# Performance work log

Measured on AMD Instinct MI355X. Metric: run time of the kernel, lower is better.

The kernel has to match this reference:

```python
import jax, jax.numpy as jnp
import numpy as np
from jax import lax

B = 32        # true batch size (groups)
C_IN = 64     # per-sample input channels
C_OUT = 64    # per-sample output channels
H = W = 256
KH = KW = 3


def setup_inputs() -> dict:
    key = jax.random.key(0)
    kx, kk = jax.random.split(key)
    # x folds the batch into channels: [1, B*C_in, H, W]
    x = jax.random.normal(kx, (1, B * C_IN, H, W), dtype=jnp.float32)
    # per-sample kernels stacked along output-filter axis: [B*C_out, C_in, kH, kW]
    kernels = jax.random.normal(kk, (B * C_OUT, C_IN, KH, KW), dtype=jnp.float32)
    return {"x": x, "kernels": kernels, "batch_size": B}


def reference(x, kernels, batch_size):
    # F.conv2d(x, kernels, stride=1, padding='same', groups=batch_size)
    # Grouped conv with feature_group_count = batch_size (one group per sample).
    out = lax.conv_general_dilated(
        x,
        kernels,
        window_strides=(1, 1),
        padding="SAME",
        feature_group_count=batch_size,
        dimension_numbers=("NCHW", "OIHW", "NCHW"),
    )
    return out
```

## Files before the change

kernel.cpp:

```cpp
#include <hip/hip_runtime.h>
#include <hip/hip_bf16.h>


typedef __bf16 bf16x8 __attribute__((ext_vector_type(8)));
typedef float  f32x4  __attribute__((ext_vector_type(4)));

#define NB 32
#define NH 256
#define NW 256
#define TILE_H 4
#define TILE_W 64
#define XROWS 6
#define XCOLS 68
#define HWSZ ((size_t)NH * NW)

__device__ __forceinline__ void gload16(const float* g, float* lds) {
    __builtin_amdgcn_global_load_lds(
        (const __attribute__((address_space(1))) unsigned int*)g,
        (__attribute__((address_space(3))) unsigned int*)lds, 16, 0, 0);
}

__global__ void repack_weights_kernel(const float* __restrict__ wsrc,
                                      __bf16* __restrict__ pk) {
    int t = blockIdx.x * blockDim.x + threadIdx.x;
    if (t >= NB * 9 * 4 * 2 * 64) return;
    int lane = t & 63;
    int r = t >> 6;
    int kc = r & 1;  r >>= 1;
    int mt = r & 3;  r >>= 2;
    int tap = r % 9;
    int b   = r / 9;
    int co  = b * 64 + mt * 16 + (lane & 15);
    int ci0 = kc * 32 + (lane >> 4) * 8;
    bf16x8 v;
#pragma unroll
    for (int j = 0; j < 8; ++j) {
        v[j] = (__bf16)wsrc[(co * 64 + ci0 + j) * 9 + tap];
    }
    *reinterpret_cast<bf16x8*>(pk + (size_t)t * 8) = v;
}

__launch_bounds__(256)
__global__ void conv_mfma_kernel(const float* __restrict__ x,
                                 const __bf16* __restrict__ pk,
                                 float* __restrict__ out) {
    __shared__ __align__(16) __bf16 xs[XROWS * XCOLS * 32];
    __shared__ __align__(16) __bf16 afs[36 * 512];

    const int orig = blockIdx.x;
    const int wg   = (orig & 7) * 1024 + (orig >> 3);
    const int b    = wg >> 8;
    const int by   = (wg >> 2) & 63;
    const int bx   = wg & 3;
    const int h0   = by * TILE_H;
    const int w0   = bx * TILE_W;

    const int tid  = threadIdx.x;
    const int wid  = tid >> 6;
    const int lane = tid & 63;
    const int nl   = lane & 15;
    const int kgrp = lane >> 4;

    const char* pkb = (const char*)(pk + (size_t)b * 9 * 4096);

    auto issue_af = [&](int kcv) {
#pragma unroll
        for (int i = 0; i < 9; ++i) {
            const int f  = wid * 9 + i;
            const int tp = f >> 2;
            const int mt = f & 3;
            const float* src = (const float*)(pkb + tp * 8192
                                              + (mt * 2 + kcv) * 1024 + lane * 16);
            gload16(src, (float*)((char*)afs + f * 1024));
        }
    };

    f32x4 acc[4][4];
#pragma unroll
    for (int mt = 0; mt < 4; ++mt)
#pragma unroll
        for (int q = 0; q < 4; ++q)
            acc[mt][q] = (f32x4){0.f, 0.f, 0.f, 0.f};

    const int c    = lane;
    const int w    = w0 - 1 + c;
    const int wcl  = min(max(w, 0), NW - 1);
    const bool wbad = (w != wcl);
    const int sciw = ((wid ^ ((c >> 1) & 3)) * 8);

    const int hr    = tid >> 3;
    const int hside = (tid >> 2) & 1;
    const int hoct  = tid & 3;
    const int hch   = 64 + hside;
    const int hw    = w0 + 63 + hside;
    const int hwc   = min(hw, NW - 1);

#pragma unroll
    for (int kc = 0; kc < 2; ++kc) {
        {
            issue_af(kc);

            const int cibase = b * 64 + kc * 32 + wid * 8;
            const float* colp = x + (size_t)cibase * HWSZ + wcl;

            float hv[8];
            if (tid < 48) {
                const int h  = h0 - 1 + hr;
                const int hc = min(max(h, 0), NH - 1);
                const float* src = x + ((size_t)(b * 64 + kc * 32 + hoct * 8) * NH + hc) * NW + hwc;
#pragma unroll
                for (int j = 0; j < 8; ++j) hv[j] = src[j * HWSZ];
                if (h != hc || hw != hwc) {
#pragma unroll
                    for (int j = 0; j < 8; ++j) hv[j] = 0.f;
                }
            }

            float va[8], vb[8];
            auto load8 = [&](int r, float* v) {
                const int h  = h0 - 1 + r;
                const int hc = min(max(h, 0), NH - 1);
                const float* src = colp + (size_t)hc * NW;
#pragma unroll
                for (int j = 0; j < 8; ++j) v[j] = src[j * HWSZ];
                if (wbad || h != hc) {
#pragma unroll
                    for (int j = 0; j < 8; ++j) v[j] = 0.f;
                }
            };
            auto store8 = [&](int r, const float* v) {
                bf16x8 o;
#pragma unroll
                for (int j = 0; j < 8; ++j) o[j] = (__bf16)v[j];
                *reinterpret_cast<bf16x8*>(xs + (r * XCOLS + c) * 32 + sciw) = o;
            };

            load8(0, va);
            load8(1, vb);
            store8(0, va); load8(2, va);
            store8(1, vb); load8(3, vb);
            store8(2, va); load8(4, va);
            store8(3, vb); load8(5, vb);
            store8(4, va);
            store8(5, vb);

            if (tid < 48) {
                bf16x8 o;
#pragma unroll
                for (int j = 0; j < 8; ++j) o[j] = (__bf16)hv[j];
                *reinterpret_cast<bf16x8*>(xs + (hr * XCOLS + hch) * 32 + hoct * 8) = o;
            }
        }
        __syncthreads();

#pragma unroll
        for (int tap = 0; tap < 9; ++tap) {
            bf16x8 afr[4];
#pragma unroll
            for (int mt = 0; mt < 4; ++mt)
                afr[mt] = *reinterpret_cast<const bf16x8*>(
                    afs + (tap * 4 + mt) * 512 + lane * 8);
            const int kh = tap / 3;
            const int kw = tap - kh * 3;
            const int rowbase = (wid + kh) * XCOLS;
#pragma unroll
            for (int q = 0; q < 4; ++q) {
                const int cc   = q * 16 + nl + kw;
                const int slot = (cc >> 1) & 3;
                bf16x8 bfv = *reinterpret_cast<const bf16x8*>(
                    xs + (rowbase + cc) * 32 + ((kgrp ^ slot) * 8));
#pragma unroll
                for (int mt = 0; mt < 4; ++mt)
                    acc[mt][q] = __builtin_amdgcn_mfma_f32_16x16x32_bf16(
                        afr[mt], bfv, acc[mt][q], 0, 0, 0);
            }
        }
        if (kc == 0) __syncthreads();
    }

    const int mrow = kgrp * 4;
    const int h = h0 + wid;
#pragma unroll
    for (int mt = 0; mt < 4; ++mt) {
#pragma unroll
        for (int q = 0; q < 4; ++q) {
            const int ww = w0 + q * 16 + nl;
#pragma unroll
            for (int rg = 0; rg < 4; ++rg) {
                const int co = mt * 16 + mrow + rg;
                out[((size_t)(b * 64 + co) * NH + h) * NW + ww] = acc[mt][q][rg];
            }
        }
    }
}

extern "C" void kernel_launch(void* const* d_in, const int* in_sizes, int n_in,
                              void* d_out, int out_size, void* d_ws, size_t ws_size,
                              hipStream_t stream) {
    const float* x = (const float*)d_in[0];
    const float* w = (const float*)d_in[1];
    float* out = (float*)d_out;
    __bf16* pk = (__bf16*)d_ws;

    {
        int total = NB * 9 * 4 * 2 * 64;
        int blk = 256;
        int grid = (total + blk - 1) / blk;
        hipLaunchKernelGGL(repack_weights_kernel, dim3(grid), dim3(blk), 0, stream,
                           w, pk);
    }
    {
        dim3 grid(8192);
        hipLaunchKernelGGL(conv_mfma_kernel, grid, dim3(256), 0, stream,
                           x, pk, out);
    }
}
```

Before: 289.4 us.

## Split each tile across 8 waves, halving per-wave output channels

```diff
diff --git a/kernel.cpp b/kernel.cpp
--- a/kernel.cpp
+++ b/kernel.cpp
@@ -11,7 +11,7 @@
 #define TILE_H 4
 #define TILE_W 64
 #define XROWS 6
-#define XCOLS 68
+#define XCOLS 66
 #define HWSZ ((size_t)NH * NW)
 
 __device__ __forceinline__ void gload16(const float* g, float* lds) {
@@ -40,7 +40,7 @@
     *reinterpret_cast<bf16x8*>(pk + (size_t)t * 8) = v;
 }
 
-__launch_bounds__(256)
+__launch_bounds__(512)
 __global__ void conv_mfma_kernel(const float* __restrict__ x,
                                  const __bf16* __restrict__ pk,
                                  float* __restrict__ out) {
@@ -60,33 +60,39 @@
     const int lane = tid & 63;
     const int nl   = lane & 15;
     const int kgrp = lane >> 4;
+    const int rloc = wid >> 1;
+    const int ch   = wid & 1;
 
     const char* pkb = (const char*)(pk + (size_t)b * 9 * 4096);
 
     auto issue_af = [&](int kcv) {
 #pragma unroll
-        for (int i = 0; i < 9; ++i) {
-            const int f  = wid * 9 + i;
-            const int tp = f >> 2;
-            const int mt = f & 3;
-            const float* src = (const float*)(pkb + tp * 8192
-                                              + (mt * 2 + kcv) * 1024 + lane * 16);
-            gload16(src, (float*)((char*)afs + f * 1024));
+        for (int i = 0; i < 5; ++i) {
+            const int f = wid + i * 8;
+            if (f < 36) {
+                const int tp = f >> 2;
+                const int mt = f & 3;
+                const float* src = (const float*)(pkb + tp * 8192
+                                                  + (mt * 2 + kcv) * 1024 + lane * 16);
+                gload16(src, (float*)((char*)afs + f * 1024));
+            }
         }
     };
 
-    f32x4 acc[4][4];
-#pragma unroll
-    for (int mt = 0; mt < 4; ++mt)
+    f32x4 acc[2][4];
+#pragma unroll
+    for (int mtl = 0; mtl < 2; ++mtl)
 #pragma unroll
         for (int q = 0; q < 4; ++q)
-            acc[mt][q] = (f32x4){0.f, 0.f, 0.f, 0.f};
-
-    const int c    = lane;
-    const int w    = w0 - 1 + c;
-    const int wcl  = min(max(w, 0), NW - 1);
+            acc[mtl][q] = (f32x4){0.f, 0.f, 0.f, 0.f};
+
+    const int c     = lane;
+    const int w     = w0 - 1 + c;
+    const int wcl   = min(max(w, 0), NW - 1);
     const bool wbad = (w != wcl);
-    const int sciw = ((wid ^ ((c >> 1) & 3)) * 8);
+    const int oct   = wid & 3;
+    const int rbase = (wid >> 2) * 3;
+    const int sciw  = ((oct ^ ((c >> 1) & 3)) * 8);
 
     const int hr    = tid >> 3;
     const int hside = (tid >> 2) & 1;
@@ -100,7 +106,7 @@
         {
             issue_af(kc);
 
-            const int cibase = b * 64 + kc * 32 + wid * 8;
+            const int cibase = b * 64 + kc * 32 + oct * 8;
             const float* colp = x + (size_t)cibase * HWSZ + wcl;
 
             float hv[8];
@@ -117,8 +123,8 @@
             }
 
             float va[8], vb[8];
-            auto load8 = [&](int r, float* v) {
-                const int h  = h0 - 1 + r;
+            auto load8 = [&](int k, float* v) {
+                const int h  = h0 - 1 + rbase + k;
                 const int hc = min(max(h, 0), NH - 1);
                 const float* src = colp + (size_t)hc * NW;
 #pragma unroll
@@ -128,21 +134,18 @@
                     for (int j = 0; j < 8; ++j) v[j] = 0.f;
                 }
             };
-            auto store8 = [&](int r, const float* v) {
+            auto store8 = [&](int k, const float* v) {
                 bf16x8 o;
 #pragma unroll
                 for (int j = 0; j < 8; ++j) o[j] = (__bf16)v[j];
-                *reinterpret_cast<bf16x8*>(xs + (r * XCOLS + c) * 32 + sciw) = o;
+                *reinterpret_cast<bf16x8*>(xs + ((rbase + k) * XCOLS + c) * 32 + sciw) = o;
             };
 
             load8(0, va);
             load8(1, vb);
             store8(0, va); load8(2, va);
-            store8(1, vb); load8(3, vb);
-            store8(2, va); load8(4, va);
-            store8(3, vb); load8(5, vb);
-            store8(4, va);
-            store8(5, vb);
+            store8(1, vb);
+            store8(2, va);
 
             if (tid < 48) {
                 bf16x8 o;
@@ -155,14 +158,14 @@
 
 #pragma unroll
         for (int tap = 0; tap < 9; ++tap) {
-            bf16x8 afr[4];
-#pragma unroll
-            for (int mt = 0; mt < 4; ++mt)
-                afr[mt] = *reinterpret_cast<const bf16x8*>(
-                    afs + (tap * 4 + mt) * 512 + lane * 8);
+            bf16x8 afr[2];
+#pragma unroll
+            for (int mtl = 0; mtl < 2; ++mtl)
+                afr[mtl] = *reinterpret_cast<const bf16x8*>(
+                    afs + (tap * 4 + ch * 2 + mtl) * 512 + lane * 8);
             const int kh = tap / 3;
             const int kw = tap - kh * 3;
-            const int rowbase = (wid + kh) * XCOLS;
+            const int rowbase = (rloc + kh) * XCOLS;
 #pragma unroll
             for (int q = 0; q < 4; ++q) {
                 const int cc   = q * 16 + nl + kw;
@@ -170,25 +173,25 @@
                 bf16x8 bfv = *reinterpret_cast<const bf16x8*>(
                     xs + (rowbase + cc) * 32 + ((kgrp ^ slot) * 8));
 #pragma unroll
-                for (int mt = 0; mt < 4; ++mt)
-                    acc[mt][q] = __builtin_amdgcn_mfma_f32_16x16x32_bf16(
-                        afr[mt], bfv, acc[mt][q], 0, 0, 0);
+                for (int mtl = 0; mtl < 2; ++mtl)
+                    acc[mtl][q] = __builtin_amdgcn_mfma_f32_16x16x32_bf16(
+                        afr[mtl], bfv, acc[mtl][q], 0, 0, 0);
             }
         }
         if (kc == 0) __syncthreads();
     }
 
     const int mrow = kgrp * 4;
-    const int h = h0 + wid;
-#pragma unroll
-    for (int mt = 0; mt < 4; ++mt) {
+    const int h = h0 + rloc;
+#pragma unroll
+    for (int mtl = 0; mtl < 2; ++mtl) {
 #pragma unroll
         for (int q = 0; q < 4; ++q) {
             const int ww = w0 + q * 16 + nl;
 #pragma unroll
             for (int rg = 0; rg < 4; ++rg) {
-                const int co = mt * 16 + mrow + rg;
-                out[((size_t)(b * 64 + co) * NH + h) * NW + ww] = acc[mt][q][rg];
+                const int co = (ch * 2 + mtl) * 16 + mrow + rg;
+                out[((size_t)(b * 64 + co) * NH + h) * NW + ww] = acc[mtl][q][rg];
             }
         }
     }
@@ -211,7 +214,7 @@
     }
     {
         dim3 grid(8192);
-        hipLaunchKernelGGL(conv_mfma_kernel, grid, dim3(256), 0, stream,
+        hipLaunchKernelGGL(conv_mfma_kernel, grid, dim3(512), 0, stream,
                            x, pk, out);
     }
 }
```

Result: slower. 336.7 us (+16.3%).
